# Kernel optimization log

Hardware: AMD Instinct MI355X
Metric: run time of the kernel (lower is better)

Reference implementation:

```python
import jax, jax.numpy as jnp
import numpy as np

N = 49920      # total nodes (128 graphs x 390 nodes)
E = 200000     # total edges
B = 128        # graphs in batch
IN_CH = 128
EDGE_DIM = 16
HEADS = 4
OUT1 = 256     # conv1 per-head out -> concat 1024
OUT2 = 64      # conv2 per-head out -> concat 256
NEG_SLOPE = 0.2


def _gatv2(x, edge_index, edge_attr, Wl, bl, Wr, br, We, att, bias, out_ch, n_nodes_total):
    """PyG GATv2Conv (concat=True, share_weights=False, eval mode).
    x: [N, F_in]; edge_index: [2, E] (row 0 = source j, row 1 = target i).
    Returns [N, HEADS*out_ch].
    """
    src, dst = edge_index[0], edge_index[1]
    xl = (x @ Wl + bl).reshape(n_nodes_total, HEADS, out_ch)  # lin_l -> source side
    xr = (x @ Wr + br).reshape(n_nodes_total, HEADS, out_ch)  # lin_r -> target side
    ef = (edge_attr @ We).reshape(-1, HEADS, out_ch)          # lin_edge (no bias)
    # per-edge GATv2 scoring: a . leaky_relu(x_j + x_i + e)
    m = jax.nn.leaky_relu(xl[src] + xr[dst] + ef, NEG_SLOPE)  # [E, H, C]
    logits = jnp.einsum('ehc,hc->eh', m, att)                 # [E, H]
    # segment softmax over incoming edges of each target node
    mx = jax.ops.segment_max(logits, dst, num_segments=n_nodes_total)
    ex = jnp.exp(logits - mx[dst])
    denom = jax.ops.segment_sum(ex, dst, num_segments=n_nodes_total)
    alpha = ex / (denom[dst] + 1e-16)                         # [E, H]
    msg = xl[src] * alpha[:, :, None]                         # [E, H, C]
    out = jax.ops.segment_sum(msg, dst, num_segments=n_nodes_total)
    return out.reshape(n_nodes_total, HEADS * out_ch) + bias


def setup_inputs() -> dict:
    key = jax.random.key(0)
    ks = jax.random.split(key, 24)
    g = lambda k, shape, fan_in: jax.random.normal(k, shape, dtype=jnp.float32) * (1.0 / np.sqrt(fan_in))
    inp = {}
    inp['x'] = jax.random.normal(ks[0], (N, IN_CH), dtype=jnp.float32)
    inp['edge_index'] = jax.random.randint(ks[1], (2, E), 0, N, dtype=jnp.int64)
    inp['edge_attr'] = jax.random.normal(ks[2], (E, EDGE_DIM), dtype=jnp.float32)
    inp['n_nodes'] = jnp.full((B,), N // B, dtype=jnp.int64)  # 390 nodes per graph
    # conv1 params
    H1 = HEADS * OUT1
    inp['Wl1'] = g(ks[3], (IN_CH, H1), IN_CH); inp['bl1'] = jnp.zeros((H1,), jnp.float32)
    inp['Wr1'] = g(ks[4], (IN_CH, H1), IN_CH); inp['br1'] = jnp.zeros((H1,), jnp.float32)
    inp['We1'] = g(ks[5], (EDGE_DIM, H1), EDGE_DIM)
    inp['att1'] = g(ks[6], (HEADS, OUT1), OUT1)
    inp['b1'] = jnp.zeros((H1,), jnp.float32)
    # conv2 params (input dim = 1024)
    H2 = HEADS * OUT2
    inp['Wl2'] = g(ks[7], (H1, H2), H1); inp['bl2'] = jnp.zeros((H2,), jnp.float32)
    inp['Wr2'] = g(ks[8], (H1, H2), H1); inp['br2'] = jnp.zeros((H2,), jnp.float32)
    inp['We2'] = g(ks[9], (EDGE_DIM, H2), EDGE_DIM)
    inp['att2'] = g(ks[10], (HEADS, OUT2), OUT2)
    inp['b2'] = jnp.zeros((H2,), jnp.float32)
    # MLP head
    inp['fc1_w'] = g(ks[11], (H2, 64), H2); inp['fc1_b'] = jnp.zeros((64,), jnp.float32)
    inp['fc2_w'] = g(ks[12], (64, 1), 64); inp['fc2_b'] = jnp.zeros((1,), jnp.float32)
    return inp


def reference(x, edge_index, edge_attr, n_nodes,
              Wl1, bl1, Wr1, br1, We1, att1, b1,
              Wl2, bl2, Wr2, br2, We2, att2, b2,
              fc1_w, fc1_b, fc2_w, fc2_b):
    h = jax.nn.relu(_gatv2(x, edge_index, edge_attr, Wl1, bl1, Wr1, br1, We1, att1, b1, OUT1, N))
    h = jax.nn.relu(_gatv2(h, edge_index, edge_attr, Wl2, bl2, Wr2, br2, We2, att2, b2, OUT2, N))
    last = jnp.cumsum(n_nodes) - 1                 # master node = last node of each graph
    master = h[last]                               # [B, 256]
    z = jax.nn.relu(master @ fc1_w + fc1_b)
    return z @ fc2_w + fc2_b                       # [B, 1]
```

## Files before the change

### kernel.cpp

```cpp
#include <hip/hip_runtime.h>
#include <hip/hip_bf16.h>
#include <cmath>

#define NN 49920
#define EE 200000
#define BB 128

typedef __attribute__((ext_vector_type(8))) short short8;
typedef __attribute__((ext_vector_type(4))) float floatx4;
typedef __attribute__((ext_vector_type(2))) float float2v;

union u8x16 { short8 v; unsigned short u[8]; };

__device__ __forceinline__ float bits2f(unsigned short u) {
    union { unsigned int i; float f; } c; c.i = ((unsigned int)u) << 16; return c.f;
}
__device__ __forceinline__ unsigned short f2bits(float f) {
    union { float f; unsigned int i; } c; c.f = f;
    unsigned int x = c.i;
    return (unsigned short)((x + 0x7fffu + ((x >> 16) & 1u)) >> 16);
}
__device__ __forceinline__ unsigned short f2bits_trunc(float f) {
    union { float f; unsigned int i; } c; c.f = f;
    return (unsigned short)(c.i >> 16);
}
__device__ __forceinline__ float2v cvt2(unsigned int w) {
    union { unsigned int i; float f; } lo, hi;
    lo.i = w << 16; hi.i = w & 0xffff0000u;
    return (float2v){lo.f, hi.f};
}
__device__ __forceinline__ float2v lrelu2(float2v v) {
    float2v t = v * 0.2f;
    return (float2v){fmaxf(v.x, t.x), fmaxf(v.y, t.y)};
}

typedef const __attribute__((address_space(1))) void* gvp;
typedef __attribute__((address_space(3))) void* lvp;
__device__ __forceinline__ void gll16(const void* g, void* l) {
    __builtin_amdgcn_global_load_lds((gvp)g, (lvp)l, 16, 0, 0);
}

__global__ void zero_int_kernel(int* __restrict__ p, int n) {
    int i = blockIdx.x * blockDim.x + threadIdx.x;
    if (i < n) p[i] = 0;
}

__global__ void convert_bf16_kernel(const float* __restrict__ src, unsigned short* __restrict__ dst, int n) {
    int i = blockIdx.x * blockDim.x + threadIdx.x;
    if (i < n) dst[i] = f2bits(src[i]);
}

__global__ void convert_weights_kernel(
    const float* __restrict__ Wl1, const float* __restrict__ Wr1,
    const float* __restrict__ Wl2, const float* __restrict__ Wr2,
    const float* __restrict__ We1, const float* __restrict__ We2,
    const float* __restrict__ bl2, const float* __restrict__ br2,
    unsigned short* __restrict__ wtl1, unsigned short* __restrict__ wtr1,
    unsigned short* __restrict__ wtlr2, unsigned short* __restrict__ weT1,
    unsigned short* __restrict__ weT2, float* __restrict__ blr2) {
    int b = blockIdx.x, tid = threadIdx.x;
    if (b < 1024) {
        const float* W = (b < 512) ? Wl1 : Wr1;
        unsigned short* WT = (b < 512) ? wtl1 : wtr1;
        int i = ((b & 511) << 8) + tid;
        int n = i >> 7, k = i & 127;
        WT[i] = f2bits(W[k * 1024 + n]);
    } else if (b < 3072) {
        int bb = b - 1024;
        const float* W = (bb < 1024) ? Wl2 : Wr2;
        int i = ((bb & 1023) << 8) + tid;
        int n = i >> 10, k = i & 1023;
        int off = (bb < 1024) ? 0 : 262144;
        wtlr2[off + i] = f2bits(W[k * 256 + n]);
    } else if (b < 3136) {
        int i = ((b - 3072) << 8) + tid;
        int col = i >> 4, k = i & 15;
        weT1[i] = f2bits(We1[k * 1024 + col]);
    } else if (b < 3152) {
        int i = ((b - 3136) << 8) + tid;
        int col = i >> 4, k = i & 15;
        weT2[i] = f2bits(We2[k * 256 + col]);
    } else {
        int i = ((b - 3152) << 8) + tid;
        if (i < 512) blr2[i] = (i < 256) ? bl2[i] : br2[i - 256];
    }
}

__global__ __launch_bounds__(256) void mfma_gemm_bt_kernel(
    const unsigned short* __restrict__ A, const unsigned short* __restrict__ WT,
    const float* __restrict__ bias, const float* __restrict__ bias2,
    unsigned short* __restrict__ C, unsigned short* __restrict__ C2,
    int M, int K, int Nout) {
    __shared__ unsigned short As[128 * 32];
    __shared__ unsigned short Bs[128 * 32];
    int tid = threadIdx.x;
    int lane = tid & 63, wid = tid >> 6;
    int gm0 = blockIdx.y * 128, gn0 = blockIdx.x * 128;
    int wm = (wid & 1) * 64, wn = (wid >> 1) * 64;
    int l15 = lane & 15, quad = lane >> 4;
    int r0 = wid * 32;
    int gr = r0 + (lane >> 2);
    int kc = (lane & 3) * 8;

    floatx4 acc[4][4];
#pragma unroll
    for (int i = 0; i < 4; i++)
#pragma unroll
        for (int j = 0; j < 4; j++)
#pragma unroll
            for (int r = 0; r < 4; r++) acc[i][j][r] = 0.f;

    const unsigned short* Ap0 = &A[(size_t)(gm0 + gr) * K + kc];
    const unsigned short* Ap1 = Ap0 + (size_t)16 * K;
    const unsigned short* Bp0 = &WT[(size_t)(gn0 + gr) * K + kc];
    const unsigned short* Bp1 = Bp0 + (size_t)16 * K;
    unsigned short* as0 = &As[r0 * 32];
    unsigned short* as1 = &As[(r0 + 16) * 32];
    unsigned short* bs0 = &Bs[r0 * 32];
    unsigned short* bs1 = &Bs[(r0 + 16) * 32];

    for (int k0 = 0; k0 < K; k0 += 32) {
        __syncthreads();
        gll16(Ap0 + k0, as0);
        gll16(Ap1 + k0, as1);
        gll16(Bp0 + k0, bs0);
        gll16(Bp1 + k0, bs1);
        __syncthreads();
        short8 af[4], bfr[4];
#pragma unroll
        for (int i = 0; i < 4; i++)
            af[i] = *(const short8*)&As[(wm + 16 * i + l15) * 32 + quad * 8];
#pragma unroll
        for (int j = 0; j < 4; j++)
            bfr[j] = *(const short8*)&Bs[(wn + 16 * j + l15) * 32 + quad * 8];
#pragma unroll
        for (int i = 0; i < 4; i++)
#pragma unroll
            for (int j = 0; j < 4; j++)
                acc[i][j] = __builtin_amdgcn_mfma_f32_16x16x32_bf16(af[i], bfr[j], acc[i][j], 0, 0, 0);
    }

    unsigned short* Cw = C;
    const float* bp = bias;
    int colb = gn0 + wn + l15;
    if (gn0 >= Nout) { Cw = C2; bp = bias2; colb -= Nout; }
#pragma unroll
    for (int i = 0; i < 4; i++) {
#pragma unroll
        for (int j = 0; j < 4; j++) {
            int col = colb + 16 * j;
            float bv = bp[col];
#pragma unroll
            for (int r = 0; r < 4; r++) {
                int rrow = gm0 + wm + 16 * i + quad * 4 + r;
                Cw[(size_t)rrow * Nout + col] = f2bits(acc[i][j][r] + bv);
            }
        }
    }
}

__global__ void hist_kernel(const int* __restrict__ ei, int* __restrict__ counts, int E) {
    int e = blockIdx.x * blockDim.x + threadIdx.x;
    if (e < E) atomicAdd(&counts[ei[E + e]], 1);
}

__global__ __launch_bounds__(256) void block_sum_kernel(
    const int* __restrict__ counts, int* __restrict__ bsum) {
    int t = threadIdx.x;
    int v = counts[blockIdx.x * 256 + t];
#pragma unroll
    for (int off = 32; off > 0; off >>= 1) v += __shfl_xor(v, off, 64);
    __shared__ int red[4];
    if ((t & 63) == 0) red[t >> 6] = v;
    __syncthreads();
    if (t == 0) bsum[blockIdx.x] = red[0] + red[1] + red[2] + red[3];
}

__global__ __launch_bounds__(256) void bsum_scan_kernel(
    const int* __restrict__ bsum, int* __restrict__ bofs,
    int* __restrict__ offsets, int NBL, int N) {
    __shared__ int tmp[256];
    int t = threadIdx.x;
    int v = (t < NBL) ? bsum[t] : 0;
    tmp[t] = v;
    __syncthreads();
    for (int off = 1; off < 256; off <<= 1) {
        int x = (t >= off) ? tmp[t - off] : 0;
        __syncthreads();
        tmp[t] += x;
        __syncthreads();
    }
    if (t < NBL) bofs[t] = tmp[t] - v;
    if (t == 255) offsets[N] = tmp[255];
}

__global__ __launch_bounds__(256) void local_scan_kernel(
    const int* __restrict__ counts, const int* __restrict__ bofs,
    int* __restrict__ offsets, int* __restrict__ woff) {
    __shared__ int tmp[256];
    int t = threadIdx.x;
    int i = blockIdx.x * 256 + t;
    int v = counts[i];
    tmp[t] = v;
    __syncthreads();
    for (int off = 1; off < 256; off <<= 1) {
        int x = (t >= off) ? tmp[t - off] : 0;
        __syncthreads();
        tmp[t] += x;
        __syncthreads();
    }
    int excl = tmp[t] - v + bofs[blockIdx.x];
    offsets[i] = excl;
    woff[i] = excl;
}

__global__ void scatter_kernel(const int* __restrict__ ei, int* __restrict__ woff,
                               int* __restrict__ perm, int* __restrict__ srcs,
                               int* __restrict__ dsts, int E) {
    int e = blockIdx.x * blockDim.x + threadIdx.x;
    if (e < E) {
        int d = ei[E + e];
        int slot = atomicAdd(&woff[d], 1);
        perm[slot] = e;
        srcs[slot] = ei[e];
        dsts[slot] = d;
    }
}

template<int HC>
__global__ __launch_bounds__(256) void edge_score_v16_kernel(
    const unsigned short* __restrict__ xl, const unsigned short* __restrict__ xr,
    int XS, const float* __restrict__ eattr, const unsigned short* __restrict__ WeT,
    const float* __restrict__ att, const int* __restrict__ perm,
    const int* __restrict__ srcs, const int* __restrict__ dsts,
    float* __restrict__ logits, int E) {
    constexpr int EB = 16;
    constexpr int CW = (HC == 1024) ? 512 : 256;
    constexpr int NP = HC / CW;
    constexpr int LDE = CW + 8;
    __shared__ unsigned short ef_s[EB * LDE];
    __shared__ int src_s[EB], dst_s[EB], e_s[16];
    __shared__ float logit_s[EB * 4];

    int tid = threadIdx.x;
    int s0 = blockIdx.x * EB;
    int lane = tid & 63, w = tid >> 6;
    int l15 = lane & 15, quad = lane >> 4;
    int hf = lane >> 5, q = lane & 31;

    if (tid < EB) { src_s[tid] = srcs[s0 + tid]; dst_s[tid] = dsts[s0 + tid]; }
    if (tid < 16) e_s[tid] = perm[s0 + tid];
    __syncthreads();

    u8x16 a;
    if (quad < 2) {
        const float* ap = &eattr[(size_t)e_s[l15] * 16 + quad * 8];
        float4 a0 = *(const float4*)ap;
        float4 a1 = *(const float4*)(ap + 4);
        a.u[0] = f2bits_trunc(a0.x); a.u[1] = f2bits_trunc(a0.y);
        a.u[2] = f2bits_trunc(a0.z); a.u[3] = f2bits_trunc(a0.w);
        a.u[4] = f2bits_trunc(a1.x); a.u[5] = f2bits_trunc(a1.y);
        a.u[6] = f2bits_trunc(a1.z); a.u[7] = f2bits_trunc(a1.w);
    } else {
#pragma unroll
        for (int j = 0; j < 8; j++) a.u[j] = 0;
    }

#pragma unroll
    for (int half = 0; half < NP; half++) {
        for (int t = w; t < CW / 16; t += 4) {
            int colg = half * CW + t * 16 + l15;
            u8x16 b;
            if (quad < 2) *(uint4*)b.u = *(const uint4*)&WeT[(size_t)colg * 16 + quad * 8];
            else {
#pragma unroll
                for (int j = 0; j < 8; j++) b.u[j] = 0;
            }
            floatx4 c = {0.f, 0.f, 0.f, 0.f};
            c = __builtin_amdgcn_mfma_f32_16x16x32_bf16(a.v, b.v, c, 0, 0, 0);
#pragma unroll
            for (int r = 0; r < 4; r++)
                ef_s[(quad * 4 + r) * LDE + t * 16 + l15] = f2bits_trunc(c[r]);
        }
        __syncthreads();

        if constexpr (HC == 1024) {
            int hloc = w >> 1;
            int head = half * 2 + hloc;
            int slot = (w & 1) * 2 + hf;
            int c0g = head * 256 + q * 8;
            int c0l = hloc * 256 + q * 8;
            float2v attv[4];
#pragma unroll
            for (int j = 0; j < 4; j++)
                attv[j] = (float2v){att[c0g + 2 * j], att[c0g + 2 * j + 1]};
            uint4 wlp[4];
#pragma unroll
            for (int pp = 0; pp < 4; pp++)
                wlp[pp] = *(const uint4*)&xl[(size_t)src_s[slot * 4 + pp] * XS + c0g];
            int prevd = -1;
            float2v r0, r1, r2, r3;
            r0 = r1 = r2 = r3 = (float2v){0.f, 0.f};
#pragma unroll
            for (int pp = 0; pp < 4; pp++) {
                int e = slot * 4 + pp;
                int d = dst_s[e];
                if (d != prevd) {
                    uint4 wr = *(const uint4*)&xr[(size_t)d * XS + c0g];
                    r0 = cvt2(wr.x); r1 = cvt2(wr.y); r2 = cvt2(wr.z); r3 = cvt2(wr.w);
                    prevd = d;
                }
                uint4 wf = *(const uint4*)&ef_s[e * LDE + c0l];
                float2v v, p2 = {0.f, 0.f};
                v = cvt2(wlp[pp].x) + r0 + cvt2(wf.x); p2 += attv[0] * lrelu2(v);
                v = cvt2(wlp[pp].y) + r1 + cvt2(wf.y); p2 += attv[1] * lrelu2(v);
                v = cvt2(wlp[pp].z) + r2 + cvt2(wf.z); p2 += attv[2] * lrelu2(v);
                v = cvt2(wlp[pp].w) + r3 + cvt2(wf.w); p2 += attv[3] * lrelu2(v);
                float part = p2.x + p2.y;
                part += __shfl_xor(part, 1, 64);
                part += __shfl_xor(part, 2, 64);
                part += __shfl_xor(part, 4, 64);
                part += __shfl_xor(part, 8, 64);
                part += __shfl_xor(part, 16, 64);
                if (q == 0) logit_s[e * 4 + head] = part;
            }
        } else {
            int c0 = q * 8;
            int hd = q >> 3;
            float2v attv[4];
#pragma unroll
            for (int j = 0; j < 4; j++)
                attv[j] = (float2v){att[c0 + 2 * j], att[c0 + 2 * j + 1]};
            uint4 wlp[2];
#pragma unroll
            for (int pp = 0; pp < 2; pp++)
                wlp[pp] = *(const uint4*)&xl[(size_t)src_s[w * 4 + hf * 2 + pp] * XS + c0];
            int prevd = -1;
            float2v r0, r1, r2, r3;
            r0 = r1 = r2 = r3 = (float2v){0.f, 0.f};
#pragma unroll
            for (int pp = 0; pp < 2; pp++) {
                int e = w * 4 + hf * 2 + pp;
                int d = dst_s[e];
                if (d != prevd) {
                    uint4 wr = *(const uint4*)&xr[(size_t)d * XS + c0];
                    r0 = cvt2(wr.x); r1 = cvt2(wr.y); r2 = cvt2(wr.z); r3 = cvt2(wr.w);
                    prevd = d;
                }
                uint4 wf = *(const uint4*)&ef_s[e * LDE + c0];
                float2v v, p2 = {0.f, 0.f};
                v = cvt2(wlp[pp].x) + r0 + cvt2(wf.x); p2 += attv[0] * lrelu2(v);
                v = cvt2(wlp[pp].y) + r1 + cvt2(wf.y); p2 += attv[1] * lrelu2(v);
                v = cvt2(wlp[pp].z) + r2 + cvt2(wf.z); p2 += attv[2] * lrelu2(v);
                v = cvt2(wlp[pp].w) + r3 + cvt2(wf.w); p2 += attv[3] * lrelu2(v);
                float part = p2.x + p2.y;
                part += __shfl_xor(part, 1, 64);
                part += __shfl_xor(part, 2, 64);
                part += __shfl_xor(part, 4, 64);
                if ((q & 7) == 0) logit_s[e * 4 + hd] = part;
            }
        }
        __syncthreads();
    }
    if (tid < EB * 4) logits[(size_t)s0 * 4 + tid] = logit_s[tid];
}

template<int HC, int WPN, bool OUT_BF16>
__global__ __launch_bounds__(256) void node_agg_wave_kernel(
    const unsigned short* __restrict__ xl, int XS, const float* __restrict__ logits,
    const int* __restrict__ srcs, const int* __restrict__ offsets,
    const float* __restrict__ bias, void* __restrict__ outv) {
    constexpr int J = HC / (64 * WPN);
    int tid = threadIdx.x;
    int wid = tid >> 6, lane = tid & 63;
    int n, ha;
    if constexpr (WPN == 2) { n = blockIdx.x * 2 + (wid >> 1); ha = wid & 1; }
    else { n = blockIdx.x * 4 + wid; ha = 0; }
    int o0 = offsets[n];
    int deg = offsets[n + 1] - o0;

    int hl;
    float m, s;
    if constexpr (WPN == 2) {
        hl = ha * 2 + (lane >> 5);
        int p = lane & 31;
        float lv = (p < deg) ? logits[(size_t)(o0 + p) * 4 + hl] : -3.0e38f;
        m = lv;
        for (int i = p + 32; i < deg; i += 32)
            m = fmaxf(m, logits[(size_t)(o0 + i) * 4 + hl]);
        m = fmaxf(m, __shfl_xor(m, 1, 64));
        m = fmaxf(m, __shfl_xor(m, 2, 64));
        m = fmaxf(m, __shfl_xor(m, 4, 64));
        m = fmaxf(m, __shfl_xor(m, 8, 64));
        m = fmaxf(m, __shfl_xor(m, 16, 64));
        s = (p < deg) ? __expf(lv - m) : 0.f;
        for (int i = p + 32; i < deg; i += 32)
            s += __expf(logits[(size_t)(o0 + i) * 4 + hl] - m);
        s += __shfl_xor(s, 1, 64);
        s += __shfl_xor(s, 2, 64);
        s += __shfl_xor(s, 4, 64);
        s += __shfl_xor(s, 8, 64);
        s += __shfl_xor(s, 16, 64);
    } else {
        hl = lane >> 4;
        int p = lane & 15;
        float lv = (p < deg) ? logits[(size_t)(o0 + p) * 4 + hl] : -3.0e38f;
        m = lv;
        for (int i = p + 16; i < deg; i += 16)
            m = fmaxf(m, logits[(size_t)(o0 + i) * 4 + hl]);
        m = fmaxf(m, __shfl_xor(m, 1, 64));
        m = fmaxf(m, __shfl_xor(m, 2, 64));
        m = fmaxf(m, __shfl_xor(m, 4, 64));
        m = fmaxf(m, __shfl_xor(m, 8, 64));
        s = (p < deg) ? __expf(lv - m) : 0.f;
        for (int i = p + 16; i < deg; i += 16)
            s += __expf(logits[(size_t)(o0 + i) * 4 + hl] - m);
        s += __shfl_xor(s, 1, 64);
        s += __shfl_xor(s, 2, 64);
        s += __shfl_xor(s, 4, 64);
        s += __shfl_xor(s, 8, 64);
    }
    float inv = 1.f / (s + 1e-16f);

    int c0 = ha * (HC / WPN) + lane * J;
    float acc[J];
#pragma unroll
    for (int v = 0; v < J; v++) acc[v] = bias[c0 + v];

    int i = 0;
    for (; i + 4 <= deg; i += 4) {
        int sl0 = o0 + i, sl1 = o0 + i + 1, sl2 = o0 + i + 2, sl3 = o0 + i + 3;
        int src0 = srcs[sl0], src1 = srcs[sl1], src2 = srcs[sl2], src3 = srcs[sl3];
        if constexpr (J == 8) {
            u8x16 a0, a1, a2, a3;
            a0.v = *(const short8*)&xl[(size_t)src0 * XS + c0];
            a1.v = *(const short8*)&xl[(size_t)src1 * XS + c0];
            a2.v = *(const short8*)&xl[(size_t)src2 * XS + c0];
            a3.v = *(const short8*)&xl[(size_t)src3 * XS + c0];
            float alpha0 = __expf(logits[(size_t)sl0 * 4 + hl] - m) * inv;
            float alpha1 = __expf(logits[(size_t)sl1 * 4 + hl] - m) * inv;
            float alpha2 = __expf(logits[(size_t)sl2 * 4 + hl] - m) * inv;
            float alpha3 = __expf(logits[(size_t)sl3 * 4 + hl] - m) * inv;
#pragma unroll
            for (int v = 0; v < 8; v++) {
                acc[v] += alpha0 * bits2f(a0.u[v]) + alpha1 * bits2f(a1.u[v]);
                acc[v] += alpha2 * bits2f(a2.u[v]) + alpha3 * bits2f(a3.u[v]);
            }
        } else {
            unsigned short u0[4], u1[4], u2[4], u3[4];
            *(ushort4*)u0 = *(const ushort4*)&xl[(size_t)src0 * XS + c0];
            *(ushort4*)u1 = *(const ushort4*)&xl[(size_t)src1 * XS + c0];
            *(ushort4*)u2 = *(const ushort4*)&xl[(size_t)src2 * XS + c0];
            *(ushort4*)u3 = *(const ushort4*)&xl[(size_t)src3 * XS + c0];
            float alpha0 = __expf(logits[(size_t)sl0 * 4 + hl] - m) * inv;
            float alpha1 = __expf(logits[(size_t)sl1 * 4 + hl] - m) * inv;
            float alpha2 = __expf(logits[(size_t)sl2 * 4 + hl] - m) * inv;
            float alpha3 = __expf(logits[(size_t)sl3 * 4 + hl] - m) * inv;
#pragma unroll
            for (int v = 0; v < 4; v++) {
                acc[v] += alpha0 * bits2f(u0[v]) + alpha1 * bits2f(u1[v]);
                acc[v] += alpha2 * bits2f(u2[v]) + alpha3 * bits2f(u3[v]);
            }
        }
    }
    for (; i + 2 <= deg; i += 2) {
        int sl0 = o0 + i, sl1 = o0 + i + 1;
        int src0 = srcs[sl0], src1 = srcs[sl1];
        const unsigned short* row0 = &xl[(size_t)src0 * XS + c0];
        const unsigned short* row1 = &xl[(size_t)src1 * XS + c0];
        float alpha0 = __expf(logits[(size_t)sl0 * 4 + hl] - m) * inv;
        float alpha1 = __expf(logits[(size_t)sl1 * 4 + hl] - m) * inv;
        if constexpr (J == 8) {
            u8x16 a0, a1;
            a0.v = *(const short8*)row0;
            a1.v = *(const short8*)row1;
#pragma unroll
            for (int v = 0; v < 8; v++) acc[v] += alpha0 * bits2f(a0.u[v]) + alpha1 * bits2f(a1.u[v]);
        } else {
            unsigned short u0[4], u1[4];
            *(ushort4*)u0 = *(const ushort4*)row0;
            *(ushort4*)u1 = *(const ushort4*)row1;
#pragma unroll
            for (int v = 0; v < 4; v++) acc[v] += alpha0 * bits2f(u0[v]) + alpha1 * bits2f(u1[v]);
        }
    }
    if (i < deg) {
        int sl = o0 + i;
        float alpha = __expf(logits[(size_t)sl * 4 + hl] - m) * inv;
        int src = srcs[sl];
        const unsigned short* row = &xl[(size_t)src * XS + c0];
        if constexpr (J == 8) {
            u8x16 a0; a0.v = *(const short8*)row;
#pragma unroll
            for (int v = 0; v < 8; v++) acc[v] += alpha * bits2f(a0.u[v]);
        } else {
            unsigned short us[4];
            *(ushort4*)us = *(const ushort4*)row;
#pragma unroll
            for (int v = 0; v < 4; v++) acc[v] += alpha * bits2f(us[v]);
        }
    }

    if constexpr (OUT_BF16) {
        unsigned short* o = (unsigned short*)outv;
        u8x16 w0;
#pragma unroll
        for (int v = 0; v < 8; v++) w0.u[v] = f2bits(fmaxf(acc[v], 0.f));
        *(short8*)&o[(size_t)n * HC + c0] = w0.v;
    } else {
        float* o = (float*)outv;
        float4 f;
        f.x = fmaxf(acc[0], 0.f); f.y = fmaxf(acc[1], 0.f);
        f.z = fmaxf(acc[2], 0.f); f.w = fmaxf(acc[3], 0.f);
        *(float4*)&o[(size_t)n * HC + c0] = f;
    }
}

__global__ __launch_bounds__(64) void mlp_head_kernel(
    const float* __restrict__ h2, const int* __restrict__ nnod,
    const float* __restrict__ w1, const float* __restrict__ b1,
    const float* __restrict__ w2, const float* __restrict__ b2,
    float* __restrict__ out, int B) {
    int b = blockIdx.x, tid = threadIdx.x;
    int sum = 0;
    for (int j = tid; j <= b; j += 64) sum += nnod[j];
#pragma unroll
    for (int off = 32; off > 0; off >>= 1) sum += __shfl_xor(sum, off, 64);
    int node = sum - 1;
    __shared__ float mast[256];
    for (int i = tid; i < 256; i += 64) mast[i] = h2[(size_t)node * 256 + i];
    __syncthreads();
    float z = 0.f;
    for (int k = 0; k < 256; k++) z += mast[k] * w1[k * 64 + tid];
    z += b1[tid];
    z = z > 0.f ? z : 0.f;
    float p = z * w2[tid];
#pragma unroll
    for (int off = 32; off > 0; off >>= 1) p += __shfl_down(p, off, 64);
    if (tid == 0) out[b] = p + b2[0];
}

extern "C" void kernel_launch(void* const* d_in, const int* in_sizes, int n_in,
                              void* d_out, int out_size, void* d_ws, size_t ws_size,
                              hipStream_t stream) {
    const float* x     = (const float*)d_in[0];
    const int*   ei    = (const int*)d_in[1];
    const float* eattr = (const float*)d_in[2];
    const int*   nnod  = (const int*)d_in[3];
    const float* Wl1 = (const float*)d_in[4];
    const float* bl1 = (const float*)d_in[5];
    const float* Wr1 = (const float*)d_in[6];
    const float* br1 = (const float*)d_in[7];
    const float* We1 = (const float*)d_in[8];
    const float* att1= (const float*)d_in[9];
    const float* b1  = (const float*)d_in[10];
    const float* Wl2 = (const float*)d_in[11];
    const float* bl2 = (const float*)d_in[12];
    const float* Wr2 = (const float*)d_in[13];
    const float* br2 = (const float*)d_in[14];
    const float* We2 = (const float*)d_in[15];
    const float* att2= (const float*)d_in[16];
    const float* b2  = (const float*)d_in[17];
    const float* fc1w= (const float*)d_in[18];
    const float* fc1b= (const float*)d_in[19];
    const float* fc2w= (const float*)d_in[20];
    const float* fc2b= (const float*)d_in[21];
    float* out = (float*)d_out;

    const int N = NN, E = EE, B = BB;
    const int NBL = N / 256;

    char* base = (char*)d_ws;
    const size_t NB1 = (size_t)N * 1024 * 2;
    unsigned short* xl1   = (unsigned short*)base;
    unsigned short* xlxr2 = (unsigned short*)base;
    float*          h2    = (float*)(base + (size_t)N * 512 * 2);
    unsigned short* xr1 = (unsigned short*)(base + NB1);
    unsigned short* h1  = (unsigned short*)(base + NB1);
    char* t = base + 2 * NB1;
    float* logits = (float*)t;        t += (size_t)E * 4 * sizeof(float);
    int* counts   = (int*)t;          t += (size_t)N * sizeof(int);
    int* offsets  = (int*)t;          t += (size_t)(N + 1) * sizeof(int);
    int* woff     = (int*)t;          t += (size_t)N * sizeof(int);
    int* perm     = (int*)t;          t += (size_t)E * sizeof(int);
    int* srcs     = (int*)t;          t += (size_t)E * sizeof(int);
    int* dsts     = (int*)t;          t += (size_t)E * sizeof(int);
    int* bsum     = (int*)t;          t += (size_t)256 * sizeof(int);
    int* bofs     = (int*)t;          t += (size_t)256 * sizeof(int);
    t = (char*)(((uintptr_t)t + 63) & ~(uintptr_t)63);
    unsigned short* xb    = (unsigned short*)t; t += (size_t)N * 128 * 2;
    unsigned short* wtl1  = (unsigned short*)t; t += (size_t)1024 * 128 * 2;
    unsigned short* wtr1  = (unsigned short*)t; t += (size_t)1024 * 128 * 2;
    unsigned short* wtlr2 = (unsigned short*)t; t += (size_t)512 * 1024 * 2;
    unsigned short* weT1  = (unsigned short*)t; t += (size_t)1024 * 16 * 2;
    unsigned short* weT2  = (unsigned short*)t; t += (size_t)256 * 16 * 2;
    float* blr2           = (float*)t;          t += (size_t)512 * sizeof(float);
    size_t required = (size_t)(t - base);
    if (ws_size < required) return;

    dim3 blk(256);

    zero_int_kernel<<<(N + 255) / 256, blk, 0, stream>>>(counts, N);
    hist_kernel<<<(E + 255) / 256, blk, 0, stream>>>(ei, counts, E);
    block_sum_kernel<<<NBL, blk, 0, stream>>>(counts, bsum);
    bsum_scan_kernel<<<1, blk, 0, stream>>>(bsum, bofs, offsets, NBL, N);
    local_scan_kernel<<<NBL, blk, 0, stream>>>(counts, bofs, offsets, woff);
    scatter_kernel<<<(E + 255) / 256, blk, 0, stream>>>(ei, woff, perm, srcs, dsts, E);

    convert_bf16_kernel<<<(N * 128 + 255) / 256, blk, 0, stream>>>(x, xb, N * 128);
    convert_weights_kernel<<<3154, blk, 0, stream>>>(Wl1, Wr1, Wl2, Wr2, We1, We2, bl2, br2,
                                                     wtl1, wtr1, wtlr2, weT1, weT2, blr2);

    {
        dim3 g1(2048 / 128, N / 128);
        mfma_gemm_bt_kernel<<<g1, blk, 0, stream>>>(xb, wtl1, bl1, br1, xl1, xr1, N, 128, 1024);
    }
    edge_score_v16_kernel<1024><<<E / 16, blk, 0, stream>>>(xl1, xr1, 1024, eattr, weT1, att1, perm, srcs, dsts, logits, E);
    node_agg_wave_kernel<1024, 2, true><<<N / 2, blk, 0, stream>>>(xl1, 1024, logits, srcs, offsets, b1, h1);

    {
        dim3 g2(512 / 128, N / 128);
        mfma_gemm_bt_kernel<<<g2, blk, 0, stream>>>(h1, wtlr2, blr2, blr2, xlxr2, xlxr2, N, 1024, 512);
    }
    edge_score_v16_kernel<256><<<E / 16, blk, 0, stream>>>(xlxr2, xlxr2 + 256, 512, eattr, weT2, att2, perm, srcs, dsts, logits, E);
    node_agg_wave_kernel<256, 1, false><<<N / 4, blk, 0, stream>>>(xlxr2, 512, logits, srcs, offsets, b2, h2);

    mlp_head_kernel<<<B, 64, 0, stream>>>(h2, nnod, fc1w, fc1b, fc2w, fc2b, out, B);
}
```

Measured before the change: 563.2 us.

## Fuse edge scoring and node aggregation into one online-softmax GAT kernel

Replaces the separate edge-score and node-aggregation kernels with one kernel per layer. Each block takes four destination nodes, computes edge features with MFMA for their CSR edge range in chunks of 16, and accumulates an online softmax with the weighted messages in registers. This removes the logits round trip through global memory, the second gather of xl rows and the dsts array. In exchange it adds per-edge serial exp/rescale work and leaves load imbalance from varying degree, including the MFMA wasted on partial chunks.

```diff
diff --git a/kernel.cpp b/kernel.cpp
--- a/kernel.cpp
+++ b/kernel.cpp
@@ -216,303 +216,206 @@
 
 __global__ void scatter_kernel(const int* __restrict__ ei, int* __restrict__ woff,
                                int* __restrict__ perm, int* __restrict__ srcs,
-                               int* __restrict__ dsts, int E) {
+                               int E) {
     int e = blockIdx.x * blockDim.x + threadIdx.x;
     if (e < E) {
         int d = ei[E + e];
         int slot = atomicAdd(&woff[d], 1);
         perm[slot] = e;
         srcs[slot] = ei[e];
-        dsts[slot] = d;
     }
 }
 
 template<int HC>
-__global__ __launch_bounds__(256) void edge_score_v16_kernel(
+__global__ __launch_bounds__(256) void fused_gat_kernel(
     const unsigned short* __restrict__ xl, const unsigned short* __restrict__ xr,
     int XS, const float* __restrict__ eattr, const unsigned short* __restrict__ WeT,
     const float* __restrict__ att, const int* __restrict__ perm,
-    const int* __restrict__ srcs, const int* __restrict__ dsts,
-    float* __restrict__ logits, int E) {
-    constexpr int EB = 16;
+    const int* __restrict__ srcs, const int* __restrict__ offsets,
+    const float* __restrict__ bias, void* __restrict__ outv) {
     constexpr int CW = (HC == 1024) ? 512 : 256;
     constexpr int NP = HC / CW;
+    constexpr int AW = (HC == 1024) ? 4 : 2;
     constexpr int LDE = CW + 8;
-    __shared__ unsigned short ef_s[EB * LDE];
-    __shared__ int src_s[EB], dst_s[EB], e_s[16];
-    __shared__ float logit_s[EB * 4];
+    __shared__ unsigned short ef_s[16 * LDE];
+    __shared__ int src_s[16], e_s[16], off_s[5];
 
     int tid = threadIdx.x;
-    int s0 = blockIdx.x * EB;
     int lane = tid & 63, w = tid >> 6;
     int l15 = lane & 15, quad = lane >> 4;
     int hf = lane >> 5, q = lane & 31;
-
-    if (tid < EB) { src_s[tid] = srcs[s0 + tid]; dst_s[tid] = dsts[s0 + tid]; }
-    if (tid < 16) e_s[tid] = perm[s0 + tid];
+    int n0 = blockIdx.x * 4;
+
+    if (tid < 5) off_s[tid] = offsets[n0 + tid];
     __syncthreads();
-
-    u8x16 a;
-    if (quad < 2) {
-        const float* ap = &eattr[(size_t)e_s[l15] * 16 + quad * 8];
-        float4 a0 = *(const float4*)ap;
-        float4 a1 = *(const float4*)(ap + 4);
-        a.u[0] = f2bits_trunc(a0.x); a.u[1] = f2bits_trunc(a0.y);
-        a.u[2] = f2bits_trunc(a0.z); a.u[3] = f2bits_trunc(a0.w);
-        a.u[4] = f2bits_trunc(a1.x); a.u[5] = f2bits_trunc(a1.y);
-        a.u[6] = f2bits_trunc(a1.z); a.u[7] = f2bits_trunc(a1.w);
+    int s0 = off_s[0];
+    int nE = off_s[4] - s0;
+
+    int node, hA = 0, c0_2 = 0;
+    if constexpr (HC == 1024) {
+        int k = w * 2 + hf;
+        node = k & 3;
+        hA = k >> 2;
     } else {
-#pragma unroll
-        for (int j = 0; j < 8; j++) a.u[j] = 0;
-    }
-
-#pragma unroll
-    for (int half = 0; half < NP; half++) {
-        for (int t = w; t < CW / 16; t += 4) {
-            int colg = half * CW + t * 16 + l15;
-            u8x16 b;
-            if (quad < 2) *(uint4*)b.u = *(const uint4*)&WeT[(size_t)colg * 16 + quad * 8];
-            else {
-#pragma unroll
-                for (int j = 0; j < 8; j++) b.u[j] = 0;
+        node = w;
+        c0_2 = lane * 4;
+    }
+    int nd = n0 + node;
+    int on0 = off_s[node] - s0;
+    int on1 = off_s[node + 1] - s0;
+
+    float m_[NP], s_[NP];
+    float2v ac[NP][AW];
+#pragma unroll
+    for (int p = 0; p < NP; p++) {
+        m_[p] = -3.0e38f; s_[p] = 0.f;
+#pragma unroll
+        for (int j = 0; j < AW; j++) ac[p][j] = (float2v){0.f, 0.f};
+    }
+
+    float2v r2v0 = {0.f, 0.f}, r2v1 = {0.f, 0.f}, at2v0 = {0.f, 0.f}, at2v1 = {0.f, 0.f};
+    if constexpr (HC == 256) {
+        uint2 wxr = *(const uint2*)&xr[(size_t)nd * XS + c0_2];
+        r2v0 = cvt2(wxr.x); r2v1 = cvt2(wxr.y);
+        at2v0 = (float2v){att[c0_2], att[c0_2 + 1]};
+        at2v1 = (float2v){att[c0_2 + 2], att[c0_2 + 3]};
+    }
+
+    for (int cs = 0; cs < nE; cs += 16) {
+        if (tid < 16) {
+            int sl = cs + tid;
+            int g = s0 + ((sl < nE) ? sl : 0);
+            src_s[tid] = srcs[g];
+            e_s[tid] = perm[g];
+        }
+        __syncthreads();
+
+        u8x16 a;
+        if (quad < 2) {
+            const float* ap = &eattr[(size_t)e_s[l15] * 16 + quad * 8];
+            float4 a0 = *(const float4*)ap;
+            float4 a1 = *(const float4*)(ap + 4);
+            a.u[0] = f2bits_trunc(a0.x); a.u[1] = f2bits_trunc(a0.y);
+            a.u[2] = f2bits_trunc(a0.z); a.u[3] = f2bits_trunc(a0.w);
+            a.u[4] = f2bits_trunc(a1.x); a.u[5] = f2bits_trunc(a1.y);
+            a.u[6] = f2bits_trunc(a1.z); a.u[7] = f2bits_trunc(a1.w);
+        } else {
+#pragma unroll
+            for (int j = 0; j < 8; j++) a.u[j] = 0;
+        }
+
+#pragma unroll
+        for (int p = 0; p < NP; p++) {
+            for (int t = w; t < CW / 16; t += 4) {
+                int colg = p * CW + t * 16 + l15;
+                u8x16 b;
+                if (quad < 2) *(uint4*)b.u = *(const uint4*)&WeT[(size_t)colg * 16 + quad * 8];
+                else {
+#pragma unroll
+                    for (int j = 0; j < 8; j++) b.u[j] = 0;
+                }
+                floatx4 c = {0.f, 0.f, 0.f, 0.f};
+                c = __builtin_amdgcn_mfma_f32_16x16x32_bf16(a.v, b.v, c, 0, 0, 0);
+#pragma unroll
+                for (int r = 0; r < 4; r++)
+                    ef_s[(quad * 4 + r) * LDE + t * 16 + l15] = f2bits_trunc(c[r]);
             }
-            floatx4 c = {0.f, 0.f, 0.f, 0.f};
-            c = __builtin_amdgcn_mfma_f32_16x16x32_bf16(a.v, b.v, c, 0, 0, 0);
-#pragma unroll
-            for (int r = 0; r < 4; r++)
-                ef_s[(quad * 4 + r) * LDE + t * 16 + l15] = f2bits_trunc(c[r]);
+            __syncthreads();
+
+            int lo = on0 > cs ? on0 : cs;
+            int hi = on1 < cs + 16 ? on1 : cs + 16;
+            if constexpr (HC == 1024) {
+                int head = hA + 2 * p;
+                int c0g = head * 256 + q * 8;
+                int c0l = hA * 256 + q * 8;
+                float2v av0 = {att[c0g], att[c0g + 1]};
+                float2v av1 = {att[c0g + 2], att[c0g + 3]};
+                float2v av2 = {att[c0g + 4], att[c0g + 5]};
+                float2v av3 = {att[c0g + 6], att[c0g + 7]};
+                uint4 wxr = *(const uint4*)&xr[(size_t)nd * XS + c0g];
+                float2v r0 = cvt2(wxr.x), r1 = cvt2(wxr.y);
+                float2v r2 = cvt2(wxr.z), r3 = cvt2(wxr.w);
+                for (int rr = lo; rr < hi; rr++) {
+                    int r = rr - cs;
+                    uint4 wx = *(const uint4*)&xl[(size_t)src_s[r] * XS + c0g];
+                    uint4 wf = *(const uint4*)&ef_s[r * LDE + c0l];
+                    float2v x0 = cvt2(wx.x), x1 = cvt2(wx.y);
+                    float2v x2 = cvt2(wx.z), x3 = cvt2(wx.w);
+                    float2v v, p2 = {0.f, 0.f};
+                    v = x0 + r0 + cvt2(wf.x); p2 += av0 * lrelu2(v);
+                    v = x1 + r1 + cvt2(wf.y); p2 += av1 * lrelu2(v);
+                    v = x2 + r2 + cvt2(wf.z); p2 += av2 * lrelu2(v);
+                    v = x3 + r3 + cvt2(wf.w); p2 += av3 * lrelu2(v);
+                    float lg = p2.x + p2.y;
+                    lg += __shfl_xor(lg, 1, 64);
+                    lg += __shfl_xor(lg, 2, 64);
+                    lg += __shfl_xor(lg, 4, 64);
+                    lg += __shfl_xor(lg, 8, 64);
+                    lg += __shfl_xor(lg, 16, 64);
+                    float mo = m_[p];
+                    float mn = fmaxf(mo, lg);
+                    float sc = __expf(mo - mn);
+                    float tt = __expf(lg - mn);
+                    m_[p] = mn;
+                    s_[p] = s_[p] * sc + tt;
+                    ac[p][0] = ac[p][0] * sc + x0 * tt;
+                    ac[p][1] = ac[p][1] * sc + x1 * tt;
+                    ac[p][2] = ac[p][2] * sc + x2 * tt;
+                    ac[p][3] = ac[p][3] * sc + x3 * tt;
+                }
+            } else {
+                for (int rr = lo; rr < hi; rr++) {
+                    int r = rr - cs;
+                    uint2 wx = *(const uint2*)&xl[(size_t)src_s[r] * XS + c0_2];
+                    uint2 wf = *(const uint2*)&ef_s[r * LDE + c0_2];
+                    float2v x0 = cvt2(wx.x), x1 = cvt2(wx.y);
+                    float2v v, p2;
+                    v = x0 + r2v0 + cvt2(wf.x); p2 = at2v0 * lrelu2(v);
+                    v = x1 + r2v1 + cvt2(wf.y); p2 += at2v1 * lrelu2(v);
+                    float lg = p2.x + p2.y;
+                    lg += __shfl_xor(lg, 1, 64);
+                    lg += __shfl_xor(lg, 2, 64);
+                    lg += __shfl_xor(lg, 4, 64);
+                    lg += __shfl_xor(lg, 8, 64);
+                    float mo = m_[0];
+                    float mn = fmaxf(mo, lg);
+                    float sc = __expf(mo - mn);
+                    float tt = __expf(lg - mn);
+                    m_[0] = mn;
+                    s_[0] = s_[0] * sc + tt;
+                    ac[0][0] = ac[0][0] * sc + x0 * tt;
+                    ac[0][1] = ac[0][1] * sc + x1 * tt;
+                }
+            }
+            __syncthreads();
         }
-        __syncthreads();
-
-        if constexpr (HC == 1024) {
-            int hloc = w >> 1;
-            int head = half * 2 + hloc;
-            int slot = (w & 1) * 2 + hf;
+    }
+
+    if constexpr (HC == 1024) {
+        unsigned short* o = (unsigned short*)outv;
+#pragma unroll
+        for (int p = 0; p < NP; p++) {
+            int head = hA + 2 * p;
             int c0g = head * 256 + q * 8;
-            int c0l = hloc * 256 + q * 8;
-            float2v attv[4];
-#pragma unroll
-            for (int j = 0; j < 4; j++)
-                attv[j] = (float2v){att[c0g + 2 * j], att[c0g + 2 * j + 1]};
-            uint4 wlp[4];
-#pragma unroll
-            for (int pp = 0; pp < 4; pp++)
-                wlp[pp] = *(const uint4*)&xl[(size_t)src_s[slot * 4 + pp] * XS + c0g];
-            int prevd = -1;
-            float2v r0, r1, r2, r3;
-            r0 = r1 = r2 = r3 = (float2v){0.f, 0.f};
-#pragma unroll
-            for (int pp = 0; pp < 4; pp++) {
-                int e = slot * 4 + pp;
-                int d = dst_s[e];
-                if (d != prevd) {
-                    uint4 wr = *(const uint4*)&xr[(size_t)d * XS + c0g];
-                    r0 = cvt2(wr.x); r1 = cvt2(wr.y); r2 = cvt2(wr.z); r3 = cvt2(wr.w);
-                    prevd = d;
-                }
-                uint4 wf = *(const uint4*)&ef_s[e * LDE + c0l];
-                float2v v, p2 = {0.f, 0.f};
-                v = cvt2(wlp[pp].x) + r0 + cvt2(wf.x); p2 += attv[0] * lrelu2(v);
-                v = cvt2(wlp[pp].y) + r1 + cvt2(wf.y); p2 += attv[1] * lrelu2(v);
-                v = cvt2(wlp[pp].z) + r2 + cvt2(wf.z); p2 += attv[2] * lrelu2(v);
-                v = cvt2(wlp[pp].w) + r3 + cvt2(wf.w); p2 += attv[3] * lrelu2(v);
-                float part = p2.x + p2.y;
-                part += __shfl_xor(part, 1, 64);
-                part += __shfl_xor(part, 2, 64);
-                part += __shfl_xor(part, 4, 64);
-                part += __shfl_xor(part, 8, 64);
-                part += __shfl_xor(part, 16, 64);
-                if (q == 0) logit_s[e * 4 + head] = part;
+            float inv = 1.f / (s_[p] + 1e-16f);
+            u8x16 wo;
+#pragma unroll
+            for (int j = 0; j < 4; j++) {
+                float2v ov = ac[p][j] * inv + (float2v){bias[c0g + 2 * j], bias[c0g + 2 * j + 1]};
+                wo.u[2 * j]     = f2bits(fmaxf(ov.x, 0.f));
+                wo.u[2 * j + 1] = f2bits(fmaxf(ov.y, 0.f));
             }
-        } else {
-            int c0 = q * 8;
-            int hd = q >> 3;
-            float2v attv[4];
-#pragma unroll
-            for (int j = 0; j < 4; j++)
-                attv[j] = (float2v){att[c0 + 2 * j], att[c0 + 2 * j + 1]};
-            uint4 wlp[2];
-#pragma unroll
-            for (int pp = 0; pp < 2; pp++)
-                wlp[pp] = *(const uint4*)&xl[(size_t)src_s[w * 4 + hf * 2 + pp] * XS + c0];
-            int prevd = -1;
-            float2v r0, r1, r2, r3;
-            r0 = r1 = r2 = r3 = (float2v){0.f, 0.f};
-#pragma unroll
-            for (int pp = 0; pp < 2; pp++) {
-                int e = w * 4 + hf * 2 + pp;
-                int d = dst_s[e];
-                if (d != prevd) {
-                    uint4 wr = *(const uint4*)&xr[(size_t)d * XS + c0];
-                    r0 = cvt2(wr.x); r1 = cvt2(wr.y); r2 = cvt2(wr.z); r3 = cvt2(wr.w);
-                    prevd = d;
-                }
-                uint4 wf = *(const uint4*)&ef_s[e * LDE + c0];
-                float2v v, p2 = {0.f, 0.f};
-                v = cvt2(wlp[pp].x) + r0 + cvt2(wf.x); p2 += attv[0] * lrelu2(v);
-                v = cvt2(wlp[pp].y) + r1 + cvt2(wf.y); p2 += attv[1] * lrelu2(v);
-                v = cvt2(wlp[pp].z) + r2 + cvt2(wf.z); p2 += attv[2] * lrelu2(v);
-                v = cvt2(wlp[pp].w) + r3 + cvt2(wf.w); p2 += attv[3] * lrelu2(v);
-                float part = p2.x + p2.y;
-                part += __shfl_xor(part, 1, 64);
-                part += __shfl_xor(part, 2, 64);
-                part += __shfl_xor(part, 4, 64);
-                if ((q & 7) == 0) logit_s[e * 4 + hd] = part;
-            }
+            *(short8*)&o[(size_t)nd * HC + c0g] = wo.v;
         }
-        __syncthreads();
-    }
-    if (tid < EB * 4) logits[(size_t)s0 * 4 + tid] = logit_s[tid];
-}
-
-template<int HC, int WPN, bool OUT_BF16>
-__global__ __launch_bounds__(256) void node_agg_wave_kernel(
-    const unsigned short* __restrict__ xl, int XS, const float* __restrict__ logits,
-    const int* __restrict__ srcs, const int* __restrict__ offsets,
-    const float* __restrict__ bias, void* __restrict__ outv) {
-    constexpr int J = HC / (64 * WPN);
-    int tid = threadIdx.x;
-    int wid = tid >> 6, lane = tid & 63;
-    int n, ha;
-    if constexpr (WPN == 2) { n = blockIdx.x * 2 + (wid >> 1); ha = wid & 1; }
-    else { n = blockIdx.x * 4 + wid; ha = 0; }
-    int o0 = offsets[n];
-    int deg = offsets[n + 1] - o0;
-
-    int hl;
-    float m, s;
-    if constexpr (WPN == 2) {
-        hl = ha * 2 + (lane >> 5);
-        int p = lane & 31;
-        float lv = (p < deg) ? logits[(size_t)(o0 + p) * 4 + hl] : -3.0e38f;
-        m = lv;
-        for (int i = p + 32; i < deg; i += 32)
-            m = fmaxf(m, logits[(size_t)(o0 + i) * 4 + hl]);
-        m = fmaxf(m, __shfl_xor(m, 1, 64));
-        m = fmaxf(m, __shfl_xor(m, 2, 64));
-        m = fmaxf(m, __shfl_xor(m, 4, 64));
-        m = fmaxf(m, __shfl_xor(m, 8, 64));
-        m = fmaxf(m, __shfl_xor(m, 16, 64));
-        s = (p < deg) ? __expf(lv - m) : 0.f;
-        for (int i = p + 32; i < deg; i += 32)
-            s += __expf(logits[(size_t)(o0 + i) * 4 + hl] - m);
-        s += __shfl_xor(s, 1, 64);
-        s += __shfl_xor(s, 2, 64);
-        s += __shfl_xor(s, 4, 64);
-        s += __shfl_xor(s, 8, 64);
-        s += __shfl_xor(s, 16, 64);
-    } else {
-        hl = lane >> 4;
-        int p = lane & 15;
-        float lv = (p < deg) ? logits[(size_t)(o0 + p) * 4 + hl] : -3.0e38f;
-        m = lv;
-        for (int i = p + 16; i < deg; i += 16)
-            m = fmaxf(m, logits[(size_t)(o0 + i) * 4 + hl]);
-        m = fmaxf(m, __shfl_xor(m, 1, 64));
-        m = fmaxf(m, __shfl_xor(m, 2, 64));
-        m = fmaxf(m, __shfl_xor(m, 4, 64));
-        m = fmaxf(m, __shfl_xor(m, 8, 64));
-        s = (p < deg) ? __expf(lv - m) : 0.f;
-        for (int i = p + 16; i < deg; i += 16)
-            s += __expf(logits[(size_t)(o0 + i) * 4 + hl] - m);
-        s += __shfl_xor(s, 1, 64);
-        s += __shfl_xor(s, 2, 64);
-        s += __shfl_xor(s, 4, 64);
-        s += __shfl_xor(s, 8, 64);
-    }
-    float inv = 1.f / (s + 1e-16f);
-
-    int c0 = ha * (HC / WPN) + lane * J;
-    float acc[J];
-#pragma unroll
-    for (int v = 0; v < J; v++) acc[v] = bias[c0 + v];
-
-    int i = 0;
-    for (; i + 4 <= deg; i += 4) {
-        int sl0 = o0 + i, sl1 = o0 + i + 1, sl2 = o0 + i + 2, sl3 = o0 + i + 3;
-        int src0 = srcs[sl0], src1 = srcs[sl1], src2 = srcs[sl2], src3 = srcs[sl3];
-        if constexpr (J == 8) {
-            u8x16 a0, a1, a2, a3;
-            a0.v = *(const short8*)&xl[(size_t)src0 * XS + c0];
-            a1.v = *(const short8*)&xl[(size_t)src1 * XS + c0];
-            a2.v = *(const short8*)&xl[(size_t)src2 * XS + c0];
-            a3.v = *(const short8*)&xl[(size_t)src3 * XS + c0];
-            float alpha0 = __expf(logits[(size_t)sl0 * 4 + hl] - m) * inv;
-            float alpha1 = __expf(logits[(size_t)sl1 * 4 + hl] - m) * inv;
-            float alpha2 = __expf(logits[(size_t)sl2 * 4 + hl] - m) * inv;
-            float alpha3 = __expf(logits[(size_t)sl3 * 4 + hl] - m) * inv;
-#pragma unroll
-            for (int v = 0; v < 8; v++) {
-                acc[v] += alpha0 * bits2f(a0.u[v]) + alpha1 * bits2f(a1.u[v]);
-                acc[v] += alpha2 * bits2f(a2.u[v]) + alpha3 * bits2f(a3.u[v]);
-            }
-        } else {
-            unsigned short u0[4], u1[4], u2[4], u3[4];
-            *(ushort4*)u0 = *(const ushort4*)&xl[(size_t)src0 * XS + c0];
-            *(ushort4*)u1 = *(const ushort4*)&xl[(size_t)src1 * XS + c0];
-            *(ushort4*)u2 = *(const ushort4*)&xl[(size_t)src2 * XS + c0];
-            *(ushort4*)u3 = *(const ushort4*)&xl[(size_t)src3 * XS + c0];
-            float alpha0 = __expf(logits[(size_t)sl0 * 4 + hl] - m) * inv;
-            float alpha1 = __expf(logits[(size_t)sl1 * 4 + hl] - m) * inv;
-            float alpha2 = __expf(logits[(size_t)sl2 * 4 + hl] - m) * inv;
-            float alpha3 = __expf(logits[(size_t)sl3 * 4 + hl] - m) * inv;
-#pragma unroll
-            for (int v = 0; v < 4; v++) {
-                acc[v] += alpha0 * bits2f(u0[v]) + alpha1 * bits2f(u1[v]);
-                acc[v] += alpha2 * bits2f(u2[v]) + alpha3 * bits2f(u3[v]);
-            }
-        }
-    }
-    for (; i + 2 <= deg; i += 2) {
-        int sl0 = o0 + i, sl1 = o0 + i + 1;
-        int src0 = srcs[sl0], src1 = srcs[sl1];
-        const unsigned short* row0 = &xl[(size_t)src0 * XS + c0];
-        const unsigned short* row1 = &xl[(size_t)src1 * XS + c0];
-        float alpha0 = __expf(logits[(size_t)sl0 * 4 + hl] - m) * inv;
-        float alpha1 = __expf(logits[(size_t)sl1 * 4 + hl] - m) * inv;
-        if constexpr (J == 8) {
-            u8x16 a0, a1;
-            a0.v = *(const short8*)row0;
-            a1.v = *(const short8*)row1;
-#pragma unroll
-            for (int v = 0; v < 8; v++) acc[v] += alpha0 * bits2f(a0.u[v]) + alpha1 * bits2f(a1.u[v]);
-        } else {
-            unsigned short u0[4], u1[4];
-            *(ushort4*)u0 = *(const ushort4*)row0;
-            *(ushort4*)u1 = *(const ushort4*)row1;
-#pragma unroll
-            for (int v = 0; v < 4; v++) acc[v] += alpha0 * bits2f(u0[v]) + alpha1 * bits2f(u1[v]);
-        }
-    }
-    if (i < deg) {
-        int sl = o0 + i;
-        float alpha = __expf(logits[(size_t)sl * 4 + hl] - m) * inv;
-        int src = srcs[sl];
-        const unsigned short* row = &xl[(size_t)src * XS + c0];
-        if constexpr (J == 8) {
-            u8x16 a0; a0.v = *(const short8*)row;
-#pragma unroll
-            for (int v = 0; v < 8; v++) acc[v] += alpha * bits2f(a0.u[v]);
-        } else {
-            unsigned short us[4];
-            *(ushort4*)us = *(const ushort4*)row;
-#pragma unroll
-            for (int v = 0; v < 4; v++) acc[v] += alpha * bits2f(us[v]);
-        }
-    }
-
-    if constexpr (OUT_BF16) {
-        unsigned short* o = (unsigned short*)outv;
-        u8x16 w0;
-#pragma unroll
-        for (int v = 0; v < 8; v++) w0.u[v] = f2bits(fmaxf(acc[v], 0.f));
-        *(short8*)&o[(size_t)n * HC + c0] = w0.v;
     } else {
         float* o = (float*)outv;
+        float inv = 1.f / (s_[0] + 1e-16f);
         float4 f;
-        f.x = fmaxf(acc[0], 0.f); f.y = fmaxf(acc[1], 0.f);
-        f.z = fmaxf(acc[2], 0.f); f.w = fmaxf(acc[3], 0.f);
-        *(float4*)&o[(size_t)n * HC + c0] = f;
+        f.x = fmaxf(ac[0][0].x * inv + bias[c0_2], 0.f);
+        f.y = fmaxf(ac[0][0].y * inv + bias[c0_2 + 1], 0.f);
+        f.z = fmaxf(ac[0][1].x * inv + bias[c0_2 + 2], 0.f);
+        f.w = fmaxf(ac[0][1].y * inv + bias[c0_2 + 3], 0.f);
+        *(float4*)&o[(size_t)nd * 256 + c0_2] = f;
     }
 }
 
@@ -597,6 +500,7 @@
     float* blr2           = (float*)t;          t += (size_t)512 * sizeof(float);
     size_t required = (size_t)(t - base);
     if (ws_size < required) return;
+    (void)logits; (void)dsts;
 
     dim3 blk(256);
 
@@ -605,7 +509,7 @@
     block_sum_kernel<<<NBL, blk, 0, stream>>>(counts, bsum);
     bsum_scan_kernel<<<1, blk, 0, stream>>>(bsum, bofs, offsets, NBL, N);
     local_scan_kernel<<<NBL, blk, 0, stream>>>(counts, bofs, offsets, woff);
-    scatter_kernel<<<(E + 255) / 256, blk, 0, stream>>>(ei, woff, perm, srcs, dsts, E);
+    scatter_kernel<<<(E + 255) / 256, blk, 0, stream>>>(ei, woff, perm, srcs, E);
 
     convert_bf16_kernel<<<(N * 128 + 255) / 256, blk, 0, stream>>>(x, xb, N * 128);
     convert_weights_kernel<<<3154, blk, 0, stream>>>(Wl1, Wr1, Wl2, Wr2, We1, We2, bl2, br2,
@@ -615,15 +519,13 @@
         dim3 g1(2048 / 128, N / 128);
         mfma_gemm_bt_kernel<<<g1, blk, 0, stream>>>(xb, wtl1, bl1, br1, xl1, xr1, N, 128, 1024);
     }
-    edge_score_v16_kernel<1024><<<E / 16, blk, 0, stream>>>(xl1, xr1, 1024, eattr, weT1, att1, perm, srcs, dsts, logits, E);
-    node_agg_wave_kernel<1024, 2, true><<<N / 2, blk, 0, stream>>>(xl1, 1024, logits, srcs, offsets, b1, h1);
+    fused_gat_kernel<1024><<<N / 4, blk, 0, stream>>>(xl1, xr1, 1024, eattr, weT1, att1, perm, srcs, offsets, b1, h1);
 
     {
         dim3 g2(512 / 128, N / 128);
         mfma_gemm_bt_kernel<<<g2, blk, 0, stream>>>(h1, wtlr2, blr2, blr2, xlxr2, xlxr2, N, 1024, 512);
     }
-    edge_score_v16_kernel<256><<<E / 16, blk, 0, stream>>>(xlxr2, xlxr2 + 256, 512, eattr, weT2, att2, perm, srcs, dsts, logits, E);
-    node_agg_wave_kernel<256, 1, false><<<N / 4, blk, 0, stream>>>(xlxr2, 512, logits, srcs, offsets, b2, h2);
+    fused_gat_kernel<256><<<N / 4, blk, 0, stream>>>(xlxr2, xlxr2 + 256, 512, eattr, weT2, att2, perm, srcs, offsets, b2, h2);
 
     mlp_head_kernel<<<B, 64, 0, stream>>>(h2, nnod, fc1w, fc1b, fc2w, fc2b, out, B);
 }
```

Measured after the change: 707.3 us. 1.26x slower.
